# Kernel tuning notes

Measured on AMD Instinct MI355X. Metric: run time of the kernel, lower is better.

The kernel has to match this reference:

```python
import jax, jax.numpy as jnp
import numpy as np


def setup_inputs() -> dict:
    key = jax.random.key(0)
    x = jax.random.normal(key, (8, 4096, 1024), dtype=jnp.float32)
    return {"x": x}


def reference(x) -> jnp.ndarray:
    # Faithful to the flax module: causal mask of zeros/-inf -> softmax ->
    # row i has uniform weights 1/(i+1) over positions 0..i, then attn @ x.
    B, T, C = x.shape
    tril = jnp.tril(jnp.ones((T, T), dtype=jnp.float32))
    attn = jnp.where(tril == 0, -jnp.inf, jnp.zeros((T, T), dtype=jnp.float32))
    attn = jax.nn.softmax(attn, axis=-1)  # [T, T], row i = 1/(i+1) on [0..i]
    # broadcast matmul over batch: [T,T] x [B,T,C] -> [B,T,C]
    return jnp.einsum('ts,bsc->btc', attn, x)
```

## Files before the change

### kernel.cpp

```cpp
#include <hip/hip_runtime.h>
#include <stdint.h>

namespace {

constexpr int kB      = 8;
constexpr int kT      = 4096;
constexpr int kC4     = 256;
constexpr int kSegLen = 64;
constexpr int kNSeg   = kT / kSegLen;
constexpr int kTiles  = kB * kNSeg;

constexpr size_t kStOff   = 256;
constexpr size_t kStWords = (size_t)kTiles * 4 * kC4;

typedef float f4 __attribute__((ext_vector_type(4)));

__device__ __forceinline__ uint64_t ld_st(const uint64_t* p) {
    return __hip_atomic_load(p, __ATOMIC_RELAXED, __HIP_MEMORY_SCOPE_AGENT);
}
__device__ __forceinline__ void st_st(uint64_t* p, uint64_t w) {
    __hip_atomic_store(p, w, __ATOMIC_RELAXED, __HIP_MEMORY_SCOPE_AGENT);
}

__global__ __launch_bounds__(256, 2) void fused_scan(const float4* __restrict__ x,
                                                     float4* __restrict__ out,
                                                     uint32_t* __restrict__ ticket,
                                                     uint64_t* __restrict__ st) {
    __shared__ uint32_t s_tile;
    if (threadIdx.x == 0) s_tile = atomicAdd(ticket, 1u);
    __syncthreads();
    const uint32_t tile = s_tile;
    const int b   = (int)(tile & 7u);
    const int seg = (int)(tile >> 3);
    const int c4  = threadIdx.x;

    const size_t base = ((size_t)(b * kT + seg * kSegLen)) * kC4 + c4;
    const float4* p = x + base;
    float sx = 0.f, sy = 0.f, sz = 0.f, sw = 0.f;
#pragma unroll 8
    for (int i = 0; i < kSegLen; ++i) {
        const float4 v = p[(size_t)i * kC4];
        sx += v.x; sy += v.y; sz += v.z; sw += v.w;
    }

    {
        const float a[4] = { sx, sy, sz, sw };
#pragma unroll
        for (int j = 0; j < 4; ++j) {
            const size_t idx = ((size_t)((b * kNSeg + seg) * 4 + j) << 8) + c4;
            st_st(st + idx, ((uint64_t)__float_as_uint(a[j]) << 32) | 1u);
        }
    }

    float ox = 0.f, oy = 0.f, oz = 0.f, ow = 0.f;
    {
        int s = 0;
        while (s < seg) {
            uint64_t v[8][4];
            bool ok = true;
#pragma unroll
            for (int k = 0; k < 8; ++k) {
                const bool in = (s + k) < seg;
#pragma unroll
                for (int j = 0; j < 4; ++j) {
                    const size_t idx =
                        ((size_t)((b * kNSeg + (s + k)) * 4 + j) << 8) + c4;
                    v[k][j] = in ? ld_st(st + idx) : (uint64_t)1u;
                }
            }
#pragma unroll
            for (int k = 0; k < 8; ++k)
#pragma unroll
                for (int j = 0; j < 4; ++j) ok &= ((uint32_t)v[k][j] != 0u);
            if (!ok) { __builtin_amdgcn_s_sleep(2); continue; }
#pragma unroll
            for (int k = 0; k < 8; ++k) {
                ox += __uint_as_float((uint32_t)(v[k][0] >> 32));
                oy += __uint_as_float((uint32_t)(v[k][1] >> 32));
                oz += __uint_as_float((uint32_t)(v[k][2] >> 32));
                ow += __uint_as_float((uint32_t)(v[k][3] >> 32));
            }
            s += 8;
        }
    }

    f4* o = (f4*)(out + base);
    const int t0 = seg * kSegLen;
#pragma unroll 4
    for (int i = 0; i < kSegLen; ++i) {
        const float4 v = p[(size_t)i * kC4];
        ox += v.x; oy += v.y; oz += v.z; ow += v.w;
        const float inv = __builtin_amdgcn_rcpf((float)(t0 + i + 1));
        f4 r;
        r.x = ox * inv; r.y = oy * inv; r.z = oz * inv; r.w = ow * inv;
        __builtin_nontemporal_store(r, o + (size_t)i * kC4);
    }
}

}

extern "C" void kernel_launch(void* const* d_in, const int* in_sizes, int n_in,
                              void* d_out, int out_size, void* d_ws, size_t ws_size,
                              hipStream_t stream) {
    const float4* x = (const float4*)d_in[0];
    float4* out     = (float4*)d_out;
    uint32_t* ctr   = (uint32_t*)d_ws;
    uint64_t* st    = (uint64_t*)((char*)d_ws + kStOff);
    (void)hipMemsetAsync(d_ws, 0, kStOff + kStWords * sizeof(uint64_t), stream);
    fused_scan<<<kTiles, 256, 0, stream>>>(x, out, ctr, st);
}
```

Before: 79.61 us.

## Split each 64-row segment across four thread groups with shared-memory prefix

Each block now uses 1024 threads, and four groups of 256 each handle 16 rows of the 64-row segment. The group partial sums are combined through shared memory. Only the first group does the decoupled-lookback over earlier segments, now unrolled 4 at a time instead of 8, and it broadcasts the carry to the other groups. This aims to shorten the serial per-thread row loops and raise memory-level parallelism. The cost is extra block barriers, and with the larger blocks fewer blocks can be resident at once for the ticketed lookback chain.

```diff
diff --git a/kernel.cpp b/kernel.cpp
--- a/kernel.cpp
+++ b/kernel.cpp
@@ -9,6 +9,7 @@
 constexpr int kSegLen = 64;
 constexpr int kNSeg   = kT / kSegLen;
 constexpr int kTiles  = kB * kNSeg;
+constexpr int kSub    = 16;
 
 constexpr size_t kStOff   = 256;
 constexpr size_t kStWords = (size_t)kTiles * 4 * kC4;
@@ -22,44 +23,55 @@
     __hip_atomic_store(p, w, __ATOMIC_RELAXED, __HIP_MEMORY_SCOPE_AGENT);
 }
 
-__global__ __launch_bounds__(256, 2) void fused_scan(const float4* __restrict__ x,
-                                                     float4* __restrict__ out,
-                                                     uint32_t* __restrict__ ticket,
-                                                     uint64_t* __restrict__ st) {
+__global__ __launch_bounds__(1024, 8) void fused_scan(const float4* __restrict__ x,
+                                                      float4* __restrict__ out,
+                                                      uint32_t* __restrict__ ticket,
+                                                      uint64_t* __restrict__ st) {
+    __shared__ float4   s_sums[4][kC4];
+    __shared__ float4   s_off[kC4];
     __shared__ uint32_t s_tile;
+
     if (threadIdx.x == 0) s_tile = atomicAdd(ticket, 1u);
     __syncthreads();
     const uint32_t tile = s_tile;
     const int b   = (int)(tile & 7u);
     const int seg = (int)(tile >> 3);
-    const int c4  = threadIdx.x;
+    const int c4  = (int)(threadIdx.x & 255u);
+    const int q   = (int)(threadIdx.x >> 8);
 
-    const size_t base = ((size_t)(b * kT + seg * kSegLen)) * kC4 + c4;
+    const size_t base = ((size_t)(b * kT + seg * kSegLen + q * kSub)) * kC4 + c4;
     const float4* p = x + base;
     float sx = 0.f, sy = 0.f, sz = 0.f, sw = 0.f;
-#pragma unroll 8
-    for (int i = 0; i < kSegLen; ++i) {
+#pragma unroll 4
+    for (int i = 0; i < kSub; ++i) {
         const float4 v = p[(size_t)i * kC4];
         sx += v.x; sy += v.y; sz += v.z; sw += v.w;
     }
+    s_sums[q][c4] = make_float4(sx, sy, sz, sw);
+    __syncthreads();
 
-    {
-        const float a[4] = { sx, sy, sz, sw };
+    float px = 0.f, py = 0.f, pz = 0.f, pw = 0.f;
+    for (int qq = 0; qq < q; ++qq) {
+        const float4 v = s_sums[qq][c4];
+        px += v.x; py += v.y; pz += v.z; pw += v.w;
+    }
+
+    if (q == 3) {
+        const float a[4] = { px + sx, py + sy, pz + sz, pw + sw };
 #pragma unroll
         for (int j = 0; j < 4; ++j) {
             const size_t idx = ((size_t)((b * kNSeg + seg) * 4 + j) << 8) + c4;
             st_st(st + idx, ((uint64_t)__float_as_uint(a[j]) << 32) | 1u);
         }
     }
-
-    float ox = 0.f, oy = 0.f, oz = 0.f, ow = 0.f;
-    {
+    if (q == 0) {
+        float ox = 0.f, oy = 0.f, oz = 0.f, ow = 0.f;
         int s = 0;
         while (s < seg) {
-            uint64_t v[8][4];
+            uint64_t v[4][4];
             bool ok = true;
 #pragma unroll
-            for (int k = 0; k < 8; ++k) {
+            for (int k = 0; k < 4; ++k) {
                 const bool in = (s + k) < seg;
 #pragma unroll
                 for (int j = 0; j < 4; ++j) {
@@ -69,25 +81,29 @@
                 }
             }
 #pragma unroll
-            for (int k = 0; k < 8; ++k)
+            for (int k = 0; k < 4; ++k)
 #pragma unroll
                 for (int j = 0; j < 4; ++j) ok &= ((uint32_t)v[k][j] != 0u);
             if (!ok) { __builtin_amdgcn_s_sleep(2); continue; }
 #pragma unroll
-            for (int k = 0; k < 8; ++k) {
+            for (int k = 0; k < 4; ++k) {
                 ox += __uint_as_float((uint32_t)(v[k][0] >> 32));
                 oy += __uint_as_float((uint32_t)(v[k][1] >> 32));
                 oz += __uint_as_float((uint32_t)(v[k][2] >> 32));
                 ow += __uint_as_float((uint32_t)(v[k][3] >> 32));
             }
-            s += 8;
+            s += 4;
         }
+        s_off[c4] = make_float4(ox, oy, oz, ow);
     }
+    __syncthreads();
 
+    const float4 co = s_off[c4];
+    float ox = co.x + px, oy = co.y + py, oz = co.z + pz, ow = co.w + pw;
     f4* o = (f4*)(out + base);
-    const int t0 = seg * kSegLen;
+    const int t0 = seg * kSegLen + q * kSub;
 #pragma unroll 4
-    for (int i = 0; i < kSegLen; ++i) {
+    for (int i = 0; i < kSub; ++i) {
         const float4 v = p[(size_t)i * kC4];
         ox += v.x; oy += v.y; oz += v.z; ow += v.w;
         const float inv = __builtin_amdgcn_rcpf((float)(t0 + i + 1));
@@ -107,5 +123,5 @@
     uint32_t* ctr   = (uint32_t*)d_ws;
     uint64_t* st    = (uint64_t*)((char*)d_ws + kStOff);
     (void)hipMemsetAsync(d_ws, 0, kStOff + kStWords * sizeof(uint64_t), stream);
-    fused_scan<<<kTiles, 256, 0, stream>>>(x, out, ctr, st);
+    fused_scan<<<kTiles, 1024, 0, stream>>>(x, out, ctr, st);
 }
```

Measured after the change: 79.34 us. No clear change (-0.3%).
